# Kernel tuning notes

Measured on AMD Instinct MI355X. Metric: run time of the kernel, lower is better.

## Reference

```python
import jax, jax.numpy as jnp
import numpy as np

N_NODES = 10000
N_EDGES = 160000
MUL0 = 128   # multiplicity of 0e in node input/output
MUL1 = 64    # multiplicity of 1o in node input/output
FC_IN = 8    # radial basis size (edge_scalar_attr dim)
FC_H = 64    # fc_neurons = [64, 64]
NUM_NEIGHBORS = 16.0
ANGLE = np.pi / 8.0
MID0 = MUL0 + MUL1   # 192 scalars in irreps_mid (simplified)
MID1 = MUL0 + MUL1   # 192 vectors (1o) in irreps_mid


def _inv_sqrt(d):
    return 1.0 / np.sqrt(d)


def setup_inputs() -> dict:
    key = jax.random.key(0)
    ks = jax.random.split(key, 18)
    rn = lambda k, shape: jax.random.normal(k, shape, dtype=jnp.float32)
    inp = {
        'node_input': rn(ks[0], (N_NODES, MUL0 + 3 * MUL1)),
        'edge_attr': rn(ks[1], (N_EDGES, 4)),            # 1x0e + 1x1o spherical harmonics
        'edge_scalar_attr': rn(ks[2], (N_EDGES, FC_IN)),
        # first Linear: node_input -> (node_features || node_self_out)
        'Wa0': rn(ks[3], (MUL0, MUL0)),   # 0e -> 0e (message branch)
        'Wa1': rn(ks[4], (MUL1, MUL1)),   # 1o -> 1o (message branch)
        'Wb0': rn(ks[5], (MUL0, MUL0)),   # 0e -> 0e (self branch)
        'Wb1': rn(ks[6], (MUL1, MUL1)),   # 1o -> 1o (self branch)
        # radial MLP
        'M1': rn(ks[7], (FC_IN, FC_H)),
        'M2': rn(ks[8], (FC_H, FC_H)),
        # per-instruction TP weight generators: [FC_H, mul] ('uvu', v=1 squeezed)
        'Wtp0': rn(ks[9], (FC_H, MUL0)),   # 0e x 0e -> 0e
        'Wtp1': rn(ks[10], (FC_H, MUL0)),  # 0e x 1o -> 1o
        'Wtp2': rn(ks[11], (FC_H, MUL1)),  # 1o x 0e -> 1o
        'Wtp3': rn(ks[12], (FC_H, MUL1)),  # 1o x 1o -> 0e
        # output Linear: irreps_mid (192x0e + 192x1o) -> 128x0e + 64x1o
        'Wo0': rn(ks[13], (MID0, MUL0)),
        'Wo1': rn(ks[14], (MID1, MUL1)),
        'edge_src': jax.random.randint(ks[15], (N_EDGES,), 0, N_NODES),
        'edge_dst': jax.random.randint(ks[16], (N_EDGES,), 0, N_NODES),
    }
    return inp


def _forward(node_input, edge_attr, edge_scalar_attr,
             Wa0, Wa1, Wb0, Wb1, M1, M2,
             Wtp0, Wtp1, Wtp2, Wtp3, Wo0, Wo1,
             edge_src, edge_dst):
    n = node_input.shape[0]
    x0 = node_input[:, :MUL0]                         # [N,128] 0e
    x1 = node_input[:, MUL0:].reshape(n, MUL1, 3)     # [N,64,3] 1o

    # Linear(node_input.irreps + irreps_node_output): split into message / self
    feat0 = (x0 @ Wa0) * _inv_sqrt(MUL0)
    feat1 = jnp.einsum('nvi,vu->nui', x1, Wa1) * _inv_sqrt(MUL1)
    self0 = (x0 @ Wb0) * _inv_sqrt(MUL0)
    self1 = jnp.einsum('nvi,vu->nui', x1, Wb1) * _inv_sqrt(MUL1)

    # gather node features to edges
    e0 = feat0[edge_src]                              # [E,128]
    e1 = feat1[edge_src]                              # [E,64,3]
    y0 = edge_attr[:, 0:1]                            # [E,1] 0e
    y1 = edge_attr[:, 1:4]                            # [E,3] 1o

    # radial MLP -> per-edge per-path 'uvu' weights (path param / sqrt(fc_out))
    h = jax.nn.gelu(edge_scalar_attr @ M1 * _inv_sqrt(FC_IN))
    h = jax.nn.gelu(h @ M2 * _inv_sqrt(FC_H))
    w0 = h @ Wtp0 * _inv_sqrt(FC_H)                   # [E,128]
    w1 = h @ Wtp1 * _inv_sqrt(FC_H)                   # [E,128]
    w2 = h @ Wtp2 * _inv_sqrt(FC_H)                   # [E,64]
    w3 = h @ Wtp3 * _inv_sqrt(FC_H)                   # [E,64]

    # CG tensor product paths (component normalization: alpha = sqrt(dim_out))
    mid0a = w0 * e0 * y0                                        # 0e x 0e -> 0e [E,128]
    mid0b = w3 * jnp.einsum('eui,ei->eu', e1, y1) * _inv_sqrt(3.0)  # 1o.1o -> 0e [E,64]
    mid1a = w1[:, :, None] * e0[:, :, None] * y1[:, None, :]   # 0e x 1o -> 1o [E,128,3]
    mid1b = w2[:, :, None] * e1 * y0[:, :, None]                # 1o x 0e -> 1o [E,64,3]

    e_cnt = edge_attr.shape[0]
    edge_mid = jnp.concatenate(
        [mid0a, mid0b, mid1a.reshape(e_cnt, -1), mid1b.reshape(e_cnt, -1)], axis=1)  # [E,768]

    # scatter-add to destination nodes, divide by sqrt(num_neighbors)
    agg = jax.ops.segment_sum(edge_mid, edge_dst, num_segments=n) * _inv_sqrt(NUM_NEIGHBORS)

    z0 = agg[:, :MID0]                                          # [N,192] 0e
    z1 = jnp.concatenate(
        [agg[:, MID0:MID0 + 3 * MUL0].reshape(n, MUL0, 3),
         agg[:, MID0 + 3 * MUL0:].reshape(n, MUL1, 3)], axis=1)  # [N,192,3] 1o

    conv0 = (z0 @ Wo0) * _inv_sqrt(MID0)
    conv1 = jnp.einsum('nvi,vu->nui', z1, Wo1) * _inv_sqrt(MID1)

    c = np.cos(ANGLE).astype(np.float32)
    s = np.sin(ANGLE).astype(np.float32)
    out0 = c * self0 + s * conv0                                 # [N,128]
    out1 = c * self1 + s * conv1                                 # [N,64,3]
    return jnp.concatenate([out0, out1.reshape(n, -1)], axis=1)  # [N,320]


def reference(node_input, edge_attr, edge_scalar_attr,
              Wa0, Wa1, Wb0, Wb1, M1, M2,
              Wtp0, Wtp1, Wtp2, Wtp3, Wo0, Wo1,
              edge_src, edge_dst):
    return _forward(node_input, edge_attr, edge_scalar_attr,
                    Wa0, Wa1, Wb0, Wb1, M1, M2,
                    Wtp0, Wtp1, Wtp2, Wtp3, Wo0, Wo1,
                    edge_src, edge_dst)
```

## Files before the change

kernel.cpp:

```cpp
#include <hip/hip_runtime.h>
#include <hip/hip_bf16.h>
#include <hip/hip_fp16.h>

#define N_NODES 10000
#define N_EDGES 160000
#define FEAT_W 320
#define CHUNK 32
#define WPE 64

typedef _Float16 half8 __attribute__((ext_vector_type(8)));
typedef float f32x4 __attribute__((ext_vector_type(4)));

__device__ __forceinline__ float gelu_tanh(float x) {
    float x3 = x * x * x;
    float t = tanhf(0.7978845608028654f * (x + 0.044715f * x3));
    return 0.5f * x * (1.0f + t);
}

__global__ __launch_bounds__(320) void node_transform(
    const float* __restrict__ node_input,
    const float* __restrict__ Wa0, const float* __restrict__ Wa1,
    const float* __restrict__ Wb0, const float* __restrict__ Wb1,
    float* __restrict__ feat_tbl, float* __restrict__ self_tbl)
{
    __shared__ __align__(16) float xT[FEAT_W][8];
    const int node0 = blockIdx.x * 8;
    const int t = threadIdx.x;
    for (int q = t; q < 640; q += 320) {
        const int n = q / 80, c4 = q - n * 80;
        const float4 v = ((const float4*)(node_input + (size_t)(node0 + n) * FEAT_W))[c4];
        xT[c4 * 4 + 0][n] = v.x; xT[c4 * 4 + 1][n] = v.y;
        xT[c4 * 4 + 2][n] = v.z; xT[c4 * 4 + 3][n] = v.w;
    }
    __syncthreads();

    float accf[8] = {0,0,0,0,0,0,0,0}, accs[8] = {0,0,0,0,0,0,0,0};
    float scale;
    if (t < 128) {
        for (int v = 0; v < 128; ++v) {
            const float wa = Wa0[v * 128 + t];
            const float wb = Wb0[v * 128 + t];
            const float4 xa = *(const float4*)&xT[v][0];
            const float4 xb = *(const float4*)&xT[v][4];
            accf[0] += xa.x * wa; accf[1] += xa.y * wa; accf[2] += xa.z * wa; accf[3] += xa.w * wa;
            accf[4] += xb.x * wa; accf[5] += xb.y * wa; accf[6] += xb.z * wa; accf[7] += xb.w * wa;
            accs[0] += xa.x * wb; accs[1] += xa.y * wb; accs[2] += xa.z * wb; accs[3] += xa.w * wb;
            accs[4] += xb.x * wb; accs[5] += xb.y * wb; accs[6] += xb.z * wb; accs[7] += xb.w * wb;
        }
        scale = 0.08838834764831845f;
    } else {
        const int r = t - 128, u = r / 3, i = r - 3 * u;
        for (int v = 0; v < 64; ++v) {
            const float wa = Wa1[v * 64 + u];
            const float wb = Wb1[v * 64 + u];
            const int row = 128 + v * 3 + i;
            const float4 xa = *(const float4*)&xT[row][0];
            const float4 xb = *(const float4*)&xT[row][4];
            accf[0] += xa.x * wa; accf[1] += xa.y * wa; accf[2] += xa.z * wa; accf[3] += xa.w * wa;
            accf[4] += xb.x * wa; accf[5] += xb.y * wa; accf[6] += xb.z * wa; accf[7] += xb.w * wa;
            accs[0] += xa.x * wb; accs[1] += xa.y * wb; accs[2] += xa.z * wb; accs[3] += xa.w * wb;
            accs[4] += xb.x * wb; accs[5] += xb.y * wb; accs[6] += xb.z * wb; accs[7] += xb.w * wb;
        }
        scale = 0.125f;
    }
#pragma unroll
    for (int n = 0; n < 8; ++n) {
        feat_tbl[(size_t)(node0 + n) * FEAT_W + t] = accf[n] * scale;
        self_tbl[(size_t)(node0 + n) * FEAT_W + t] = accs[n] * scale;
    }
}

__global__ __launch_bounds__(256) void mlp_kernel(
    const float* __restrict__ esa,
    const float* __restrict__ M1,
    const float* __restrict__ M2,
    const int* __restrict__ edge_dst,
    float* __restrict__ h2buf,
    int* __restrict__ counts)
{
    __shared__ __align__(16) float sh[4][64];
    const int wave = threadIdx.x >> 6;
    const int lane = threadIdx.x & 63;
    const int e = blockIdx.x * 4 + wave;

    if (lane == 0) atomicAdd(&counts[edge_dst[e]], 1);

    const float4 e0 = ((const float4*)(esa + (size_t)e * 8))[0];
    const float4 e1 = ((const float4*)(esa + (size_t)e * 8))[1];
    float h = e0.x * M1[0 * 64 + lane] + e0.y * M1[1 * 64 + lane]
            + e0.z * M1[2 * 64 + lane] + e0.w * M1[3 * 64 + lane]
            + e1.x * M1[4 * 64 + lane] + e1.y * M1[5 * 64 + lane]
            + e1.z * M1[6 * 64 + lane] + e1.w * M1[7 * 64 + lane];
    h = gelu_tanh(h * 0.35355339059327373f);
    sh[wave][lane] = h;
    __syncthreads();

    float h2 = 0.f;
    const float4* shp = (const float4*)sh[wave];
#pragma unroll
    for (int q = 0; q < 16; ++q) {
        const float4 s = shp[q];
        h2 += s.x * M2[(4 * q + 0) * 64 + lane];
        h2 += s.y * M2[(4 * q + 1) * 64 + lane];
        h2 += s.z * M2[(4 * q + 2) * 64 + lane];
        h2 += s.w * M2[(4 * q + 3) * 64 + lane];
    }
    h2 = gelu_tanh(h2 * 0.125f);
    h2buf[(size_t)e * 64 + lane] = h2;
}

__global__ __launch_bounds__(1024) void scan_kernel(
    const int* __restrict__ counts, int* __restrict__ offsets, int* __restrict__ cursor)
{
    __shared__ int wsum[16];
    const int wid = threadIdx.x >> 6, lane = threadIdx.x & 63;
    int base = 0;
    for (int c = 0; c < 10; ++c) {
        const int i = c * 1024 + threadIdx.x;
        const int v = (i < N_NODES) ? counts[i] : 0;
        int x = v;
#pragma unroll
        for (int off = 1; off < 64; off <<= 1) {
            int y = __shfl_up(x, off, 64);
            if (lane >= off) x += y;
        }
        if (lane == 63) wsum[wid] = x;
        __syncthreads();
        if (threadIdx.x < 16) {
            int s = wsum[threadIdx.x];
#pragma unroll
            for (int off = 1; off < 16; off <<= 1) {
                int y = __shfl_up(s, off, 64);
                if ((int)threadIdx.x >= off) s += y;
            }
            wsum[threadIdx.x] = s;
        }
        __syncthreads();
        const int waveoff = (wid == 0) ? 0 : wsum[wid - 1];
        const int excl = base + waveoff + x - v;
        if (i < N_NODES) { offsets[i] = excl; cursor[i] = excl; }
        const int tot = wsum[15];
        __syncthreads();
        base += tot;
    }
    if (threadIdx.x == 0) offsets[N_NODES] = base;
}

__global__ void fill_kernel(const int* __restrict__ edge_dst,
                            const int* __restrict__ edge_src,
                            const float* __restrict__ edge_attr,
                            int* __restrict__ cursor, int* __restrict__ elist,
                            int* __restrict__ srcs_csr, float* __restrict__ y4csr) {
    int e = blockIdx.x * 256 + threadIdx.x;
    if (e < N_EDGES) {
        int pos = atomicAdd(&cursor[edge_dst[e]], 1);
        elist[pos] = e;
        srcs_csr[pos] = edge_src[e];
        ((float4*)y4csr)[pos] = ((const float4*)edge_attr)[e];
    }
}

__global__ __launch_bounds__(256) void wproj_kernel(
    const int* __restrict__ elist,
    const float* __restrict__ h2buf,
    const float* __restrict__ Wtp0,
    const float* __restrict__ Wtp1,
    const float* __restrict__ Wtp2,
    const float* __restrict__ Wtp3,
    __half* __restrict__ wbuf)
{
    const int wave = threadIdx.x >> 6;
    const int lane = threadIdx.x & 63;
    const int quad = lane >> 4;
    const int n16 = lane & 15;
    const int pbase = blockIdx.x * WPE;
    const int colbase = wave * 96;

    half8 bf[6][2];
#pragma unroll
    for (int c = 0; c < 6; ++c) {
        const int col = colbase + c * 16 + n16;
        const float* src; int stride;
        if (col < 128)      { src = Wtp0 + col;         stride = 128; }
        else if (col < 256) { src = Wtp1 + (col - 128); stride = 128; }
        else if (col < 320) { src = Wtp2 + (col - 256); stride = 64;  }
        else                { src = Wtp3 + (col - 320); stride = 64;  }
#pragma unroll
        for (int s = 0; s < 2; ++s)
#pragma unroll
            for (int j = 0; j < 8; ++j)
                bf[c][s][j] = (_Float16)src[(s * 32 + quad * 8 + j) * stride];
    }

    for (int g = 0; g < 4; ++g) {
        const int eid = elist[pbase + g * 16 + n16];
        const float* hrow = h2buf + (size_t)eid * 64;
        half8 af[2];
#pragma unroll
        for (int s = 0; s < 2; ++s) {
            const float4 p0 = *(const float4*)(hrow + s * 32 + quad * 8);
            const float4 p1 = *(const float4*)(hrow + s * 32 + quad * 8 + 4);
            af[s][0] = (_Float16)p0.x; af[s][1] = (_Float16)p0.y;
            af[s][2] = (_Float16)p0.z; af[s][3] = (_Float16)p0.w;
            af[s][4] = (_Float16)p1.x; af[s][5] = (_Float16)p1.y;
            af[s][6] = (_Float16)p1.z; af[s][7] = (_Float16)p1.w;
        }
#pragma unroll
        for (int c = 0; c < 6; ++c) {
            f32x4 acc = {0.f, 0.f, 0.f, 0.f};
            acc = __builtin_amdgcn_mfma_f32_16x16x32_f16(af[0], bf[c][0], acc, 0, 0, 0);
            acc = __builtin_amdgcn_mfma_f32_16x16x32_f16(af[1], bf[c][1], acc, 0, 0, 0);
#pragma unroll
            for (int r = 0; r < 4; ++r) {
                const int edge = g * 16 + quad * 4 + r;
                wbuf[(size_t)(pbase + edge) * 384 + colbase + c * 16 + n16] =
                    (__half)(acc[r] * 0.125f);
            }
        }
    }
}

__global__ __launch_bounds__(384) void gather_kernel(
    const int* __restrict__ offsets,
    const int* __restrict__ srcs_csr,
    const float* __restrict__ y4csr,
    const __half* __restrict__ wbuf,
    const float* __restrict__ feat_tbl,
    const float* __restrict__ self_tbl,
    const float* __restrict__ Wo0,
    const float* __restrict__ Wo1,
    float* __restrict__ out)
{
    __shared__ __align__(16) __half wsh[CHUNK * 384];
    __shared__ float ys[CHUNK][4];
    __shared__ int   srcs[CHUNK];
    __shared__ float z[768];

    const int node = blockIdx.x;
    const int t = threadIdx.x;

    int f0;
    if (t < 128)      f0 = t;
    else if (t < 256) f0 = t - 128;
    else if (t < 320) f0 = 128 + 3 * (t - 256);
    else              f0 = 128 + 3 * (t - 320);

    float acc = 0.f, acc3a = 0.f, acc3b = 0.f, acc3c = 0.f;
    const int beg = offsets[node], end = offsets[node + 1];

    for (int cb = beg; cb < end; cb += CHUNK) {
        const int ne = min(CHUNK, end - cb);
        if (t < ne) {
            srcs[t] = srcs_csr[cb + t];
            ((float4*)ys)[t] = ((const float4*)y4csr)[cb + t];
        }
        for (int q = t; q < ne * 48; q += 384)
            ((float4*)wsh)[q] = ((const float4*)(wbuf + (size_t)cb * 384))[q];
        __syncthreads();

        if (t < 128) {
            for (int e = 0; e < ne; ++e) {
                const float w = __half2float(wsh[e * 384 + t]);
                const float* fr = feat_tbl + (size_t)srcs[e] * FEAT_W;
                acc += w * fr[f0] * ys[e][0];
            }
        } else if (t < 256) {
            for (int e = 0; e < ne; ++e) {
                const float w = __half2float(wsh[e * 384 + t]);
                const float* fr = feat_tbl + (size_t)srcs[e] * FEAT_W;
                const float p = w * fr[f0];
                acc3a += p * ys[e][1];
                acc3b += p * ys[e][2];
                acc3c += p * ys[e][3];
            }
        } else if (t < 320) {
            for (int e = 0; e < ne; ++e) {
                const float w = __half2float(wsh[e * 384 + t]);
                const float* fr = feat_tbl + (size_t)srcs[e] * FEAT_W;
                const float p = w * ys[e][0];
                acc3a += p * fr[f0];
                acc3b += p * fr[f0 + 1];
                acc3c += p * fr[f0 + 2];
            }
        } else {
            for (int e = 0; e < ne; ++e) {
                const float w = __half2float(wsh[e * 384 + t]);
                const float* fr = feat_tbl + (size_t)srcs[e] * FEAT_W;
                const float d = fr[f0] * ys[e][1] + fr[f0 + 1] * ys[e][2]
                              + fr[f0 + 2] * ys[e][3];
                acc += w * d;
            }
        }
        __syncthreads();
    }

    const float sZ = 0.25f;
    if (t < 128) {
        z[t] = acc * sZ;
    } else if (t < 256) {
        const int u = t - 128;
        z[192 + 0 * 192 + u] = acc3a * sZ;
        z[192 + 1 * 192 + u] = acc3b * sZ;
        z[192 + 2 * 192 + u] = acc3c * sZ;
    } else if (t < 320) {
        const int u = t - 256;
        z[192 + 0 * 192 + 128 + u] = acc3a * sZ;
        z[192 + 1 * 192 + 128 + u] = acc3b * sZ;
        z[192 + 2 * 192 + 128 + u] = acc3c * sZ;
    } else {
        z[128 + (t - 320)] = acc * sZ * 0.5773502691896258f;
    }
    __syncthreads();

    const float sA = 0.07216878364870323f;
    const float cR = 0.92387953251128674f;
    const float sR = 0.38268343236508978f;

    if (t < 128) {
        float conv = 0.f;
        const float4* z4 = (const float4*)z;
#pragma unroll 8
        for (int q = 0; q < 48; ++q) {
            const float4 zz = z4[q];
            conv += zz.x * Wo0[(4 * q + 0) * 128 + t];
            conv += zz.y * Wo0[(4 * q + 1) * 128 + t];
            conv += zz.z * Wo0[(4 * q + 2) * 128 + t];
            conv += zz.w * Wo0[(4 * q + 3) * 128 + t];
        }
        const float sv = self_tbl[(size_t)node * FEAT_W + t];
        out[(size_t)node * FEAT_W + t] = cR * sv + sR * conv * sA;
    } else if (t < 320) {
        const int idx = t - 128;
        const int i = idx >> 6, u = idx & 63;
        float conv = 0.f;
        const float4* z4 = (const float4*)(z + 192 + i * 192);
#pragma unroll 8
        for (int q = 0; q < 48; ++q) {
            const float4 zz = z4[q];
            conv += zz.x * Wo1[(4 * q + 0) * 64 + u];
            conv += zz.y * Wo1[(4 * q + 1) * 64 + u];
            conv += zz.z * Wo1[(4 * q + 2) * 64 + u];
            conv += zz.w * Wo1[(4 * q + 3) * 64 + u];
        }
        const int col = 128 + u * 3 + i;
        const float sv = self_tbl[(size_t)node * FEAT_W + col];
        out[(size_t)node * FEAT_W + col] = cR * sv + sR * conv * sA;
    }
}

extern "C" void kernel_launch(void* const* d_in, const int* in_sizes, int n_in,
                              void* d_out, int out_size, void* d_ws, size_t ws_size,
                              hipStream_t stream) {
    const float* node_input = (const float*)d_in[0];
    const float* edge_attr  = (const float*)d_in[1];
    const float* esa        = (const float*)d_in[2];
    const float* Wa0  = (const float*)d_in[3];
    const float* Wa1  = (const float*)d_in[4];
    const float* Wb0  = (const float*)d_in[5];
    const float* Wb1  = (const float*)d_in[6];
    const float* M1   = (const float*)d_in[7];
    const float* M2   = (const float*)d_in[8];
    const float* Wtp0 = (const float*)d_in[9];
    const float* Wtp1 = (const float*)d_in[10];
    const float* Wtp2 = (const float*)d_in[11];
    const float* Wtp3 = (const float*)d_in[12];
    const float* Wo0  = (const float*)d_in[13];
    const float* Wo1  = (const float*)d_in[14];
    const int* edge_src = (const int*)d_in[15];
    const int* edge_dst = (const int*)d_in[16];
    float* out = (float*)d_out;

    float*  feat_tbl = (float*)d_ws;
    float*  self_tbl = feat_tbl + (size_t)N_NODES * FEAT_W;
    float*  h2buf    = self_tbl + (size_t)N_NODES * FEAT_W;
    float*  y4csr    = h2buf + (size_t)N_EDGES * 64;
    int*    counts   = (int*)(y4csr + (size_t)N_EDGES * 4);
    int*    offsets  = counts + N_NODES;
    int*    cursor   = offsets + N_NODES + 1;
    int*    elist    = cursor + N_NODES;
    int*    srcs_csr = elist + N_EDGES;
    __half* wbuf     = (__half*)(srcs_csr + N_EDGES);

    hipMemsetAsync(counts, 0, sizeof(int) * N_NODES, stream);

    node_transform<<<N_NODES / 8, 320, 0, stream>>>(node_input, Wa0, Wa1, Wb0, Wb1,
                                                    feat_tbl, self_tbl);
    mlp_kernel<<<N_EDGES / 4, 256, 0, stream>>>(esa, M1, M2, edge_dst, h2buf, counts);
    scan_kernel<<<1, 1024, 0, stream>>>(counts, offsets, cursor);
    fill_kernel<<<N_EDGES / 256, 256, 0, stream>>>(edge_dst, edge_src, edge_attr,
                                                   cursor, elist, srcs_csr, y4csr);
    wproj_kernel<<<N_EDGES / WPE, 256, 0, stream>>>(
        elist, h2buf, Wtp0, Wtp1, Wtp2, Wtp3, wbuf);
    gather_kernel<<<N_NODES, 384, 0, stream>>>(offsets, srcs_csr, y4csr, wbuf,
                                               feat_tbl, self_tbl, Wo0, Wo1, out);
}
```

Measured before the change: 412.9 us.

## Fuse per-edge TP weight projection into gather kernel via in-block MFMA

Result: no change. 407.2 us (-1.4%).

```diff
diff --git a/kernel.cpp b/kernel.cpp
--- a/kernel.cpp
+++ b/kernel.cpp
@@ -6,7 +6,6 @@
 #define N_EDGES 160000
 #define FEAT_W 320
 #define CHUNK 32
-#define WPE 64
 
 typedef _Float16 half8 __attribute__((ext_vector_type(8)));
 typedef float f32x4 __attribute__((ext_vector_type(4)));
@@ -75,7 +74,7 @@
     const float* __restrict__ M1,
     const float* __restrict__ M2,
     const int* __restrict__ edge_dst,
-    float* __restrict__ h2buf,
+    __half* __restrict__ h2buf,
     int* __restrict__ counts)
 {
     __shared__ __align__(16) float sh[4][64];
@@ -106,7 +105,31 @@
         h2 += s.w * M2[(4 * q + 3) * 64 + lane];
     }
     h2 = gelu_tanh(h2 * 0.125f);
-    h2buf[(size_t)e * 64 + lane] = h2;
+    h2buf[(size_t)e * 64 + lane] = (__half)(h2 * 0.125f);
+}
+
+__global__ __launch_bounds__(256) void pack_wtp(
+    const float* __restrict__ Wtp0, const float* __restrict__ Wtp1,
+    const float* __restrict__ Wtp2, const float* __restrict__ Wtp3,
+    __half* __restrict__ wtp_pack)
+{
+    const int gid = blockIdx.x * 256 + threadIdx.x;
+    if (gid >= 24 * 64) return;
+    const int lane = gid & 63;
+    const int tile = gid >> 6;
+    const int quad = lane >> 4, n16 = lane & 15;
+    const int col = tile * 16 + n16;
+    const float* src; int stride;
+    if (col < 128)      { src = Wtp0 + col;         stride = 128; }
+    else if (col < 256) { src = Wtp1 + (col - 128); stride = 128; }
+    else if (col < 320) { src = Wtp2 + (col - 256); stride = 64;  }
+    else                { src = Wtp3 + (col - 320); stride = 64;  }
+    __half* dst = wtp_pack + (size_t)gid * 16;
+#pragma unroll
+    for (int s = 0; s < 2; ++s)
+#pragma unroll
+        for (int j = 0; j < 8; ++j)
+            dst[s * 8 + j] = (__half)src[(s * 32 + quad * 8 + j) * stride];
 }
 
 __global__ __launch_bounds__(1024) void scan_kernel(
@@ -160,71 +183,13 @@
     }
 }
 
-__global__ __launch_bounds__(256) void wproj_kernel(
-    const int* __restrict__ elist,
-    const float* __restrict__ h2buf,
-    const float* __restrict__ Wtp0,
-    const float* __restrict__ Wtp1,
-    const float* __restrict__ Wtp2,
-    const float* __restrict__ Wtp3,
-    __half* __restrict__ wbuf)
-{
-    const int wave = threadIdx.x >> 6;
-    const int lane = threadIdx.x & 63;
-    const int quad = lane >> 4;
-    const int n16 = lane & 15;
-    const int pbase = blockIdx.x * WPE;
-    const int colbase = wave * 96;
-
-    half8 bf[6][2];
-#pragma unroll
-    for (int c = 0; c < 6; ++c) {
-        const int col = colbase + c * 16 + n16;
-        const float* src; int stride;
-        if (col < 128)      { src = Wtp0 + col;         stride = 128; }
-        else if (col < 256) { src = Wtp1 + (col - 128); stride = 128; }
-        else if (col < 320) { src = Wtp2 + (col - 256); stride = 64;  }
-        else                { src = Wtp3 + (col - 320); stride = 64;  }
-#pragma unroll
-        for (int s = 0; s < 2; ++s)
-#pragma unroll
-            for (int j = 0; j < 8; ++j)
-                bf[c][s][j] = (_Float16)src[(s * 32 + quad * 8 + j) * stride];
-    }
-
-    for (int g = 0; g < 4; ++g) {
-        const int eid = elist[pbase + g * 16 + n16];
-        const float* hrow = h2buf + (size_t)eid * 64;
-        half8 af[2];
-#pragma unroll
-        for (int s = 0; s < 2; ++s) {
-            const float4 p0 = *(const float4*)(hrow + s * 32 + quad * 8);
-            const float4 p1 = *(const float4*)(hrow + s * 32 + quad * 8 + 4);
-            af[s][0] = (_Float16)p0.x; af[s][1] = (_Float16)p0.y;
-            af[s][2] = (_Float16)p0.z; af[s][3] = (_Float16)p0.w;
-            af[s][4] = (_Float16)p1.x; af[s][5] = (_Float16)p1.y;
-            af[s][6] = (_Float16)p1.z; af[s][7] = (_Float16)p1.w;
-        }
-#pragma unroll
-        for (int c = 0; c < 6; ++c) {
-            f32x4 acc = {0.f, 0.f, 0.f, 0.f};
-            acc = __builtin_amdgcn_mfma_f32_16x16x32_f16(af[0], bf[c][0], acc, 0, 0, 0);
-            acc = __builtin_amdgcn_mfma_f32_16x16x32_f16(af[1], bf[c][1], acc, 0, 0, 0);
-#pragma unroll
-            for (int r = 0; r < 4; ++r) {
-                const int edge = g * 16 + quad * 4 + r;
-                wbuf[(size_t)(pbase + edge) * 384 + colbase + c * 16 + n16] =
-                    (__half)(acc[r] * 0.125f);
-            }
-        }
-    }
-}
-
 __global__ __launch_bounds__(384) void gather_kernel(
     const int* __restrict__ offsets,
+    const int* __restrict__ elist,
     const int* __restrict__ srcs_csr,
     const float* __restrict__ y4csr,
-    const __half* __restrict__ wbuf,
+    const __half* __restrict__ h2buf,
+    const __half* __restrict__ wtp_pack,
     const float* __restrict__ feat_tbl,
     const float* __restrict__ self_tbl,
     const float* __restrict__ Wo0,
@@ -232,12 +197,23 @@
     float* __restrict__ out)
 {
     __shared__ __align__(16) __half wsh[CHUNK * 384];
+    __shared__ __align__(16) __half h2s[CHUNK * 64];
     __shared__ float ys[CHUNK][4];
     __shared__ int   srcs[CHUNK];
     __shared__ float z[768];
 
     const int node = blockIdx.x;
     const int t = threadIdx.x;
+    const int wave = t >> 6, lane = t & 63;
+    const int quad = lane >> 4, n16 = lane & 15;
+
+    half8 bf[4][2];
+#pragma unroll
+    for (int c = 0; c < 4; ++c) {
+        const __half* p = wtp_pack + (size_t)((wave * 4 + c) * 64 + lane) * 16;
+        bf[c][0] = *(const half8*)p;
+        bf[c][1] = *(const half8*)(p + 8);
+    }
 
     int f0;
     if (t < 128)      f0 = t;
@@ -254,8 +230,33 @@
             srcs[t] = srcs_csr[cb + t];
             ((float4*)ys)[t] = ((const float4*)y4csr)[cb + t];
         }
-        for (int q = t; q < ne * 48; q += 384)
-            ((float4*)wsh)[q] = ((const float4*)(wbuf + (size_t)cb * 384))[q];
+        for (int q = t; q < ne * 8; q += 384) {
+            const int eL = q >> 3, u = q & 7;
+            const half8 hv = ((const half8*)(h2buf + (size_t)elist[cb + eL] * 64))[u];
+            *(half8*)((char*)h2s + eL * 128 + ((u * 16) ^ ((eL & 7) << 4))) = hv;
+        }
+        __syncthreads();
+
+#pragma unroll
+        for (int g = 0; g < 2; ++g) {
+            if (g * 16 < ne) {
+                const int e = g * 16 + n16;
+                const char* hb = (const char*)h2s + e * 128;
+                const int sw = (e & 7) << 4;
+                const half8 af0 = *(const half8*)(hb + ((quad * 16) ^ sw));
+                const half8 af1 = *(const half8*)(hb + ((64 + quad * 16) ^ sw));
+#pragma unroll
+                for (int c = 0; c < 4; ++c) {
+                    f32x4 acc4 = {0.f, 0.f, 0.f, 0.f};
+                    acc4 = __builtin_amdgcn_mfma_f32_16x16x32_f16(af0, bf[c][0], acc4, 0, 0, 0);
+                    acc4 = __builtin_amdgcn_mfma_f32_16x16x32_f16(af1, bf[c][1], acc4, 0, 0, 0);
+                    const int col = (wave * 4 + c) * 16 + n16;
+#pragma unroll
+                    for (int r = 0; r < 4; ++r)
+                        wsh[(g * 16 + quad * 4 + r) * 384 + col] = (__half)acc4[r];
+                }
+            }
+        }
         __syncthreads();
 
         if (t < 128) {
@@ -372,25 +373,25 @@
 
     float*  feat_tbl = (float*)d_ws;
     float*  self_tbl = feat_tbl + (size_t)N_NODES * FEAT_W;
-    float*  h2buf    = self_tbl + (size_t)N_NODES * FEAT_W;
-    float*  y4csr    = h2buf + (size_t)N_EDGES * 64;
+    __half* h2buf    = (__half*)(self_tbl + (size_t)N_NODES * FEAT_W);
+    float*  y4csr    = (float*)(h2buf + (size_t)N_EDGES * 64);
     int*    counts   = (int*)(y4csr + (size_t)N_EDGES * 4);
     int*    offsets  = counts + N_NODES;
     int*    cursor   = offsets + N_NODES + 1;
     int*    elist    = cursor + N_NODES;
     int*    srcs_csr = elist + N_EDGES;
-    __half* wbuf     = (__half*)(srcs_csr + N_EDGES);
+    __half* wtp_pack = (__half*)(srcs_csr + N_EDGES);
 
     hipMemsetAsync(counts, 0, sizeof(int) * N_NODES, stream);
 
+    pack_wtp<<<6, 256, 0, stream>>>(Wtp0, Wtp1, Wtp2, Wtp3, wtp_pack);
     node_transform<<<N_NODES / 8, 320, 0, stream>>>(node_input, Wa0, Wa1, Wb0, Wb1,
                                                     feat_tbl, self_tbl);
     mlp_kernel<<<N_EDGES / 4, 256, 0, stream>>>(esa, M1, M2, edge_dst, h2buf, counts);
     scan_kernel<<<1, 1024, 0, stream>>>(counts, offsets, cursor);
     fill_kernel<<<N_EDGES / 256, 256, 0, stream>>>(edge_dst, edge_src, edge_attr,
                                                    cursor, elist, srcs_csr, y4csr);
-    wproj_kernel<<<N_EDGES / WPE, 256, 0, stream>>>(
-        elist, h2buf, Wtp0, Wtp1, Wtp2, Wtp3, wbuf);
-    gather_kernel<<<N_NODES, 384, 0, stream>>>(offsets, srcs_csr, y4csr, wbuf,
-                                               feat_tbl, self_tbl, Wo0, Wo1, out);
-}
+    gather_kernel<<<N_NODES, 384, 0, stream>>>(offsets, elist, srcs_csr, y4csr,
+                                               h2buf, wtp_pack, feat_tbl, self_tbl,
+                                               Wo0, Wo1, out);
+}
```
